# Performance work log

Hardware: AMD Instinct MI355X
Metric: run time of the kernel (lower is better)

## Reference

```python
import jax, jax.numpy as jnp
import numpy as np

DIM = 2048; H = 16; DK = 128; DV = 128; SEQ = 2048; KCONV = 4
KEY_DIM = H * DK; VAL_DIM = H * DV
EPS_L2 = 1e-6; EPS_RMS = 1e-6; SP_THRESH = 20.0


def setup_inputs() -> dict:
    key = jax.random.key(0)
    ks = jax.random.split(key, 20)
    f = jnp.float32
    def w(k, shape, scale):
        return jax.random.normal(k, shape, f) * scale
    s_in = DIM ** -0.5
    return {
        "x": jax.random.normal(ks[0], (1, SEQ, DIM), f),
        "ve": jax.random.normal(ks[1], (1, SEQ, H, DV), f),
        "sa_lambdas": jnp.array([0.7, 0.3], f),
        "Wq": w(ks[2], (DIM, KEY_DIM), s_in),
        "Wk": w(ks[3], (DIM, KEY_DIM), s_in),
        "Wv": w(ks[4], (DIM, VAL_DIM), s_in),
        "conv_q": w(ks[5], (KEY_DIM, KCONV), 0.5),
        "conv_k": w(ks[6], (KEY_DIM, KCONV), 0.5),
        "conv_v": w(ks[7], (VAL_DIM, KCONV), 0.5),
        "Wf1": w(ks[8], (DIM, DV), s_in),
        "Wf2": w(ks[9], (DV, KEY_DIM), DV ** -0.5),
        "Wb": w(ks[10], (DIM, H), s_in),
        "A_log": jnp.log(jax.random.uniform(ks[11], (H,), f, 1.0, 16.0)),
        "dt_bias": jnp.zeros((KEY_DIM,), f),
        "Wg1": w(ks[12], (DIM, DV), s_in),
        "Wg2": w(ks[13], (DV, VAL_DIM), DV ** -0.5),
        "bg2": jnp.zeros((VAL_DIM,), f),
        "norm_w": jnp.ones((DV,), f),
        "Wo": w(ks[14], (VAL_DIM, DIM), VAL_DIM ** -0.5),
    }


def _short_conv_silu(u, w):
    # u: [b, s, c], w: [c, K]; causal depthwise conv + silu
    s = u.shape[1]
    up = jnp.pad(u, ((0, 0), (w.shape[1] - 1, 0), (0, 0)))
    y = sum(up[:, i:i + s, :] * w[:, i] for i in range(w.shape[1]))
    return jax.nn.silu(y)


def _l2norm(t):
    return t * jax.lax.rsqrt(jnp.sum(t * t, axis=-1, keepdims=True) + EPS_L2)


def _forward(x, ve, sa_lambdas, Wq, Wk, Wv, conv_q, conv_k, conv_v,
             Wf1, Wf2, Wb, A_log, dt_bias, Wg1, Wg2, bg2, norm_w, Wo):
    b, s, _ = x.shape  # b == 1
    q = _short_conv_silu(x @ Wq, conv_q).reshape(b, s, H, DK)
    k = _short_conv_silu(x @ Wk, conv_k).reshape(b, s, H, DK)
    v = _short_conv_silu(x @ Wv, conv_v).reshape(b, s, H, DV)
    v = sa_lambdas[0] * v + sa_lambdas[1] * ve
    # KDA gate: per-(head, key-dim) log decay
    g = ((x @ Wf1) @ Wf2).reshape(b, s, H, DK) + dt_bias.reshape(H, DK)
    sp = jnp.where(g > SP_THRESH, g, jnp.log1p(jnp.exp(jnp.minimum(g, SP_THRESH))))
    glog = -jnp.exp(A_log)[None, None, :, None] * sp  # [b,s,h,dk]
    beta = jax.nn.sigmoid(x @ Wb)  # [b,s,h]
    # l2-normalize q,k; scale q by dk^-0.5 (chunk_kda default scale)
    qn = _l2norm(q) * (DK ** -0.5)
    kn = _l2norm(k)
    # gated delta-rule recurrence over time (b==1, squeeze batch)
    def step(S, inp):
        qt, kt, vt, gt, bt = inp  # [h,dk],[h,dk],[h,dv],[h,dk],[h]
        S = S * jnp.exp(gt)[..., None]  # per-key-channel decay
        pred = jnp.einsum('hk,hkv->hv', kt, S)
        vt_new = bt[:, None] * (vt - pred)
        S = S + kt[:, :, None] * vt_new[:, None, :]
        ot = jnp.einsum('hk,hkv->hv', qt, S)
        return S, ot
    S0 = jnp.zeros((H, DK, DV), x.dtype)
    _, o = jax.lax.scan(step, S0, (qn[0], kn[0], v[0], glog[0], beta[0]))
    o = o[None]  # [1,s,h,dv]
    # sigmoid-gated RMSNorm over head_v_dim
    gate = ((x @ Wg1) @ Wg2 + bg2).reshape(b, s, H, DV)
    var = jnp.mean(o * o, axis=-1, keepdims=True)
    o = o * jax.lax.rsqrt(var + EPS_RMS) * norm_w
    o = o * jax.nn.sigmoid(gate)
    return o.reshape(b, s, VAL_DIM) @ Wo  # [1,s,dim]


def reference(x, ve, sa_lambdas, Wq, Wk, Wv, conv_q, conv_k, conv_v,
              Wf1, Wf2, Wb, A_log, dt_bias, Wg1, Wg2, bg2, norm_w, Wo):
    return _forward(x, ve, sa_lambdas, Wq, Wk, Wv, conv_q, conv_k, conv_v,
                    Wf1, Wf2, Wb, A_log, dt_bias, Wg1, Wg2, bg2, norm_w, Wo)
```

## Files before the change

### kernel.cpp

```cpp
#include <hip/hip_runtime.h>
#include <hip/hip_bf16.h>
#include <stdint.h>
#include <stddef.h>

#define SEQL 2048
#define DIMSZ 2048
#define HN 16
#define DKD 128
#define DVD 128
#define QSCALE 0.08838834764831843f

typedef __attribute__((ext_vector_type(4))) float f32x4;
typedef __attribute__((ext_vector_type(2))) float f32x2;
typedef __attribute__((ext_vector_type(8))) short bf16x8;

__device__ __forceinline__ float sigmoid_f(float x) { return 1.f / (1.f + __expf(-x)); }

#define BM 128
#define BN 128
#define BKK 64

__global__ __launch_bounds__(256) void gemm_bt(
    const __hip_bfloat16* __restrict__ A, const __hip_bfloat16* __restrict__ B,
    float* __restrict__ C, int M, int N, int lda, int ldb, int klen, int accum)
{
  __shared__ __hip_bfloat16 As[BM * BKK];
  __shared__ __hip_bfloat16 Bs[BN * BKK];
  const int tid = threadIdx.x;
  const int lane = tid & 63;
  const int w = tid >> 6;
  const int wm = w >> 1, wn = w & 1;
  const int m0 = blockIdx.y * BM, n0 = blockIdx.x * BN;
  const int l15 = lane & 15, l4 = lane >> 4;
  const int kbase = blockIdx.z * klen;

  f32x4 acc[4][4] = {};

  for (int k0 = kbase; k0 < kbase + klen; k0 += BKK) {
#pragma unroll
    for (int i = 0; i < 4; ++i) {
      const int c = (w * 4 + i) * 64 + lane;
      const int row = c >> 3;
      const int colb = (c & 7) * 8;
      __builtin_amdgcn_global_load_lds(
          (const __attribute__((address_space(1))) void*)(A + (size_t)(m0 + row) * lda + k0 + colb),
          (__attribute__((address_space(3))) void*)(As + (size_t)c * 8), 16, 0, 0);
      __builtin_amdgcn_global_load_lds(
          (const __attribute__((address_space(1))) void*)(B + (size_t)(n0 + row) * ldb + k0 + colb),
          (__attribute__((address_space(3))) void*)(Bs + (size_t)c * 8), 16, 0, 0);
    }
    __syncthreads();
#pragma unroll
    for (int kk = 0; kk < BKK; kk += 32) {
      bf16x8 af[4], bfv[4];
#pragma unroll
      for (int mi = 0; mi < 4; ++mi)
        af[mi] = *(const bf16x8*)(As + (wm * 64 + mi * 16 + l15) * BKK + kk + l4 * 8);
#pragma unroll
      for (int ni = 0; ni < 4; ++ni)
        bfv[ni] = *(const bf16x8*)(Bs + (wn * 64 + ni * 16 + l15) * BKK + kk + l4 * 8);
#pragma unroll
      for (int mi = 0; mi < 4; ++mi)
#pragma unroll
        for (int ni = 0; ni < 4; ++ni)
          acc[mi][ni] = __builtin_amdgcn_mfma_f32_16x16x32_bf16(af[mi], bfv[ni], acc[mi][ni], 0, 0, 0);
    }
    __syncthreads();
  }

  float* Cz = C + (size_t)blockIdx.z * M * N;
#pragma unroll
  for (int mi = 0; mi < 4; ++mi) {
#pragma unroll
    for (int ni = 0; ni < 4; ++ni) {
      const int row = m0 + wm * 64 + mi * 16 + l4 * 4;
      const int col = n0 + wn * 64 + ni * 16 + l15;
#pragma unroll
      for (int r = 0; r < 4; ++r) {
        size_t idx = (size_t)(row + r) * N + col;
        if (accum) Cz[idx] += acc[mi][ni][r];
        else Cz[idx] = acc[mi][ni][r];
      }
    }
  }
}

#define PHASE256(MQ, NQ, NEEDA, NEEDB)                                          \
  {                                                                             \
    if (NEEDA) {                                                                \
      _Pragma("unroll") for (int m2 = 0; m2 < 4; ++m2)                          \
      _Pragma("unroll") for (int ks = 0; ks < 2; ++ks) {                        \
        const int la = (MQ) * 128 + wm * 64 + m2 * 16 + l15;                    \
        const int kc = ks * 4 + l4;                                             \
        a[m2][ks] = *(const bf16x8*)(lds + cb + la * 64 + (kc ^ (la & 7)) * 8); \
      }                                                                         \
    }                                                                           \
    if (NEEDB) {                                                                \
      _Pragma("unroll") for (int n2 = 0; n2 < 2; ++n2)                          \
      _Pragma("unroll") for (int ks = 0; ks < 2; ++ks) {                        \
        const int lb = (NQ) * 128 + wn * 32 + n2 * 16 + l15;                    \
        const int kc = ks * 4 + l4;                                             \
        b[n2][ks] = *(const bf16x8*)(lds + cb + 16384 + lb * 64 + (kc ^ (lb & 7)) * 8); \
      }                                                                         \
    }                                                                           \
    __builtin_amdgcn_s_setprio(1);                                              \
    _Pragma("unroll") for (int m2 = 0; m2 < 4; ++m2)                            \
    _Pragma("unroll") for (int n2 = 0; n2 < 2; ++n2)                            \
    _Pragma("unroll") for (int ks = 0; ks < 2; ++ks)                            \
      acc[(MQ) * 4 + m2][(NQ) * 2 + n2] = __builtin_amdgcn_mfma_f32_16x16x32_bf16( \
          a[m2][ks], b[n2][ks], acc[(MQ) * 4 + m2][(NQ) * 2 + n2], 0, 0, 0);    \
    __builtin_amdgcn_s_setprio(0);                                              \
  }

__global__ __launch_bounds__(512, 2) void gemm_bt256(
    const __hip_bfloat16* __restrict__ A, const __hip_bfloat16* __restrict__ B,
    float* __restrict__ C, int M, int N, int lda, int ldb, int NT)
{
  __shared__ __hip_bfloat16 lds[65536];
  const int tid = threadIdx.x;
  const int w = tid >> 6, lane = tid & 63;
  const int wm = w >> 2, wn = w & 3;
  const int l15 = lane & 15, l4 = lane >> 4;
  const int m0 = blockIdx.y * 256, n0 = blockIdx.x * 256;

  f32x4 acc[8][4] = {};
  bf16x8 a[4][2], b[2][2];

  auto stage_half = [&](int which, int t1) {
    const int buf = t1 & 1;
    const int k0n = ((t1 < NT) ? t1 : 0) * 64;
    const int mat = which & 1;
    const int half = which >> 1;
#pragma unroll
    for (int i = 0; i < 2; ++i) {
      const int c = i * 512 + tid;
      const int l = half * 128 + (c >> 3);
      const int kcs = (c & 7) ^ (l & 7);
      const __hip_bfloat16* src;
      if (mat == 0) {
        const int grow = ((l >> 6) & 1) * 128 + (l >> 7) * 64 + (l & 63);
        src = A + (size_t)(m0 + grow) * lda + k0n + kcs * 8;
      } else {
        const int gcol = ((l >> 5) & 3) * 64 + (l >> 7) * 32 + (l & 31);
        src = B + (size_t)(n0 + gcol) * ldb + k0n + kcs * 8;
      }
      __builtin_amdgcn_global_load_lds(
          (const __attribute__((address_space(1))) void*)src,
          (__attribute__((address_space(3))) void*)(lds + (size_t)buf * 32768 + mat * 16384 + half * 8192 + (size_t)c * 8),
          16, 0, 0);
    }
  };

  stage_half(0, 0); stage_half(1, 0); stage_half(2, 0); stage_half(3, 0);

  for (int t = 0; t < NT; ++t) {
    const size_t cb = (size_t)(t & 1) * 32768;
    stage_half(0, t + 1);
    asm volatile("s_waitcnt vmcnt(6)" ::: "memory");
    __builtin_amdgcn_s_barrier();
    __builtin_amdgcn_sched_barrier(0);
    PHASE256(0, 0, 1, 1)
    __builtin_amdgcn_s_barrier();
    stage_half(1, t + 1);
    asm volatile("s_waitcnt vmcnt(4)" ::: "memory");
    __builtin_amdgcn_s_barrier();
    __builtin_amdgcn_sched_barrier(0);
    PHASE256(0, 1, 0, 1)
    __builtin_amdgcn_s_barrier();
    stage_half(2, t + 1);
    __builtin_amdgcn_s_barrier();
    __builtin_amdgcn_sched_barrier(0);
    PHASE256(1, 1, 1, 0)
    __builtin_amdgcn_s_barrier();
    stage_half(3, t + 1);
    __builtin_amdgcn_s_barrier();
    __builtin_amdgcn_sched_barrier(0);
    PHASE256(1, 0, 0, 1)
    __builtin_amdgcn_s_barrier();
  }
  asm volatile("s_waitcnt vmcnt(0)" ::: "memory");

#pragma unroll
  for (int mi = 0; mi < 8; ++mi) {
#pragma unroll
    for (int ni = 0; ni < 4; ++ni) {
      const int row = m0 + wm * 128 + mi * 16 + l4 * 4;
      const int col = n0 + wn * 64 + ni * 16 + l15;
#pragma unroll
      for (int r = 0; r < 4; ++r)
        C[(size_t)(row + r) * N + col] = acc[mi][ni][r];
    }
  }
}

__global__ __launch_bounds__(256) void gemm_btsplit(
    const __hip_bfloat16* __restrict__ Ah, const __hip_bfloat16* __restrict__ Al,
    const __hip_bfloat16* __restrict__ Bh, const __hip_bfloat16* __restrict__ Bl,
    float* __restrict__ C, int M, int N, int lda, int ldb, int klen)
{
  __shared__ __hip_bfloat16 Ash[BM * BKK];
  __shared__ __hip_bfloat16 Asl[BM * BKK];
  __shared__ __hip_bfloat16 Bsh[BN * BKK];
  __shared__ __hip_bfloat16 Bsl[BN * BKK];
  const int tid = threadIdx.x;
  const int lane = tid & 63;
  const int w = tid >> 6;
  const int wm = w >> 1, wn = w & 1;
  const int m0 = blockIdx.y * BM, n0 = blockIdx.x * BN;
  const int l15 = lane & 15, l4 = lane >> 4;
  const int kbase = blockIdx.z * klen;

  f32x4 acc[4][4] = {};

  for (int k0 = kbase; k0 < kbase + klen; k0 += BKK) {
#pragma unroll
    for (int i = 0; i < 4; ++i) {
      const int c = (w * 4 + i) * 64 + lane;
      const int row = c >> 3;
      const int colb = (c & 7) * 8;
      const size_t go = (size_t)(m0 + row) * lda + k0 + colb;
      const size_t gn = (size_t)(n0 + row) * ldb + k0 + colb;
      __builtin_amdgcn_global_load_lds(
          (const __attribute__((address_space(1))) void*)(Ah + go),
          (__attribute__((address_space(3))) void*)(Ash + (size_t)c * 8), 16, 0, 0);
      __builtin_amdgcn_global_load_lds(
          (const __attribute__((address_space(1))) void*)(Al + go),
          (__attribute__((address_space(3))) void*)(Asl + (size_t)c * 8), 16, 0, 0);
      __builtin_amdgcn_global_load_lds(
          (const __attribute__((address_space(1))) void*)(Bh + gn),
          (__attribute__((address_space(3))) void*)(Bsh + (size_t)c * 8), 16, 0, 0);
      __builtin_amdgcn_global_load_lds(
          (const __attribute__((address_space(1))) void*)(Bl + gn),
          (__attribute__((address_space(3))) void*)(Bsl + (size_t)c * 8), 16, 0, 0);
    }
    __syncthreads();
#pragma unroll
    for (int kk = 0; kk < BKK; kk += 32) {
      bf16x8 afh[4], afl[4], bfh[4], bfl[4];
#pragma unroll
      for (int mi = 0; mi < 4; ++mi) {
        const int ao = (wm * 64 + mi * 16 + l15) * BKK + kk + l4 * 8;
        afh[mi] = *(const bf16x8*)(Ash + ao);
        afl[mi] = *(const bf16x8*)(Asl + ao);
      }
#pragma unroll
      for (int ni = 0; ni < 4; ++ni) {
        const int bo = (wn * 64 + ni * 16 + l15) * BKK + kk + l4 * 8;
        bfh[ni] = *(const bf16x8*)(Bsh + bo);
        bfl[ni] = *(const bf16x8*)(Bsl + bo);
      }
#pragma unroll
      for (int mi = 0; mi < 4; ++mi)
#pragma unroll
        for (int ni = 0; ni < 4; ++ni) {
          acc[mi][ni] = __builtin_amdgcn_mfma_f32_16x16x32_bf16(afh[mi], bfh[ni], acc[mi][ni], 0, 0, 0);
          acc[mi][ni] = __builtin_amdgcn_mfma_f32_16x16x32_bf16(afh[mi], bfl[ni], acc[mi][ni], 0, 0, 0);
          acc[mi][ni] = __builtin_amdgcn_mfma_f32_16x16x32_bf16(afl[mi], bfh[ni], acc[mi][ni], 0, 0, 0);
        }
    }
    __syncthreads();
  }

  float* Cz = C + (size_t)blockIdx.z * M * N;
#pragma unroll
  for (int mi = 0; mi < 4; ++mi) {
#pragma unroll
    for (int ni = 0; ni < 4; ++ni) {
      const int row = m0 + wm * 64 + mi * 16 + l4 * 4;
      const int col = n0 + wn * 64 + ni * 16 + l15;
#pragma unroll
      for (int r = 0; r < 4; ++r)
        Cz[(size_t)(row + r) * N + col] = acc[mi][ni][r];
    }
  }
}

__global__ __launch_bounds__(256) void transpose_cast_kernel(
    const float* __restrict__ in, __hip_bfloat16* __restrict__ outT,
    __hip_bfloat16* __restrict__ outLo, int R, int C)
{
  __shared__ float tile[32][33];
  const int c0 = blockIdx.x * 32, r0 = blockIdx.y * 32;
  const int tc = threadIdx.x & 31, tr = threadIdx.x >> 5;
#pragma unroll
  for (int i = 0; i < 4; ++i)
    tile[tr + i * 8][tc] = in[(size_t)(r0 + tr + i * 8) * C + c0 + tc];
  __syncthreads();
#pragma unroll
  for (int i = 0; i < 4; ++i) {
    float val = tile[tc][tr + i * 8];
    __hip_bfloat16 h = __float2bfloat16(val);
    size_t oi = (size_t)(c0 + tr + i * 8) * R + r0 + tc;
    outT[oi] = h;
    if (outLo) outLo[oi] = __float2bfloat16(val - __bfloat162float(h));
  }
}

__global__ __launch_bounds__(256) void cast_split_kernel(
    const float* __restrict__ in, __hip_bfloat16* __restrict__ hi,
    __hip_bfloat16* __restrict__ lo, int n4)
{
  int idx = blockIdx.x * 256 + threadIdx.x;
  if (idx >= n4) return;
  f32x4 v = *(const f32x4*)(in + (size_t)idx * 4);
  union { __hip_bfloat16 b[4]; unsigned long long u; } ph, pl;
#pragma unroll
  for (int j = 0; j < 4; ++j) {
    float f = v[j];
    __hip_bfloat16 hh = __float2bfloat16(f);
    ph.b[j] = hh;
    pl.b[j] = __float2bfloat16(f - __bfloat162float(hh));
  }
  *(unsigned long long*)((char*)hi + (size_t)idx * 8) = ph.u;
  if (lo) *(unsigned long long*)((char*)lo + (size_t)idx * 8) = pl.u;
}

__global__ __launch_bounds__(256) void reduce8_kernel(
    const float* __restrict__ part, __hip_bfloat16* __restrict__ hi,
    __hip_bfloat16* __restrict__ lo, int n4, size_t chunk)
{
  int idx = blockIdx.x * 256 + threadIdx.x;
  if (idx >= n4) return;
  f32x4 a = *(const f32x4*)(part + (size_t)idx * 4);
#pragma unroll
  for (int z = 1; z < 8; ++z) {
    f32x4 b = *(const f32x4*)(part + z * chunk + (size_t)idx * 4);
    a.x += b.x; a.y += b.y; a.z += b.z; a.w += b.w;
  }
  union { __hip_bfloat16 b[4]; unsigned long long u; } ph, pl;
#pragma unroll
  for (int j = 0; j < 4; ++j) {
    float f = a[j];
    __hip_bfloat16 hh = __float2bfloat16(f);
    ph.b[j] = hh;
    pl.b[j] = __float2bfloat16(f - __bfloat162float(hh));
  }
  *(unsigned long long*)((char*)hi + (size_t)idx * 8) = ph.u;
  if (lo) *(unsigned long long*)((char*)lo + (size_t)idx * 8) = pl.u;
}

__global__ __launch_bounds__(256) void beta_kernel(
    const float* __restrict__ x, const float* __restrict__ Wb, float* __restrict__ betaT)
{
  int idx = blockIdx.x * 256 + threadIdx.x;
  int s = idx >> 4, h = idx & 15;
  const float* xr = x + (size_t)s * DIMSZ;
  float acc = 0.f;
  for (int d = 0; d < DIMSZ; d += 4) {
    f32x4 xv = *(const f32x4*)(xr + d);
    acc = fmaf(xv.x, Wb[(size_t)(d + 0) * HN + h], acc);
    acc = fmaf(xv.y, Wb[(size_t)(d + 1) * HN + h], acc);
    acc = fmaf(xv.z, Wb[(size_t)(d + 2) * HN + h], acc);
    acc = fmaf(xv.w, Wb[(size_t)(d + 3) * HN + h], acc);
  }
  betaT[(size_t)h * SEQL + s] = 1.f / (1.f + expf(-acc));
}

#define SL20(r, d) ((r) * 160 + ((d) >> 4) * 20 + ((d) & 15))

__global__ __launch_bounds__(256) void kda_pref(
    const float* __restrict__ qkv, const float* __restrict__ ve,
    const float* __restrict__ lam,
    const float* __restrict__ cwq, const float* __restrict__ cwk, const float* __restrict__ cwv,
    const float* __restrict__ gbuf,
    const float* __restrict__ dtb, const float* __restrict__ A_log,
    const float* __restrict__ betaT,
    __hip_bfloat16* __restrict__ Xgh, __hip_bfloat16* __restrict__ KTh,
    float* __restrict__ uvS, float* __restrict__ olocS, float* __restrict__ Pg)
{
  __shared__ float GL2[32 * 160];
  __shared__ float kL2[32 * 160];
  __shared__ float qL2[32 * 132];
  __shared__ float vL2[32 * 128];
  __shared__ float ALB[32][33];
  __shared__ float Bdiag[32], betaL[32];
  __shared__ float csumW[4 * 128];

  const int bid = blockIdx.x;
  const int h = bid >> 6, cc = bid & 63;
  const int tid = threadIdx.x;
  const int w = tid >> 6, lane = tid & 63;
  const size_t hc = (size_t)h * 64 + cc;
  const float Aexp = __expf(A_log[h]);

  {
    const int c = lane * 2;
    const int r0g = cc * 32 + w * 8;
    const int cg = h * 128 + c;

    f32x4 wq0 = *(const f32x4*)(cwq + (size_t)cg * 4), wq1 = *(const f32x4*)(cwq + (size_t)(cg + 1) * 4);
    f32x4 wk0 = *(const f32x4*)(cwk + (size_t)cg * 4), wk1 = *(const f32x4*)(cwk + (size_t)(cg + 1) * 4);
    f32x4 wv0 = *(const f32x4*)(cwv + (size_t)cg * 4), wv1 = *(const f32x4*)(cwv + (size_t)(cg + 1) * 4);
    f32x2 dt2 = *(const f32x2*)(dtb + cg);
    const float l0 = lam[0], l1 = lam[1];

    f32x2 xqr[11], xkr[11], xvr[11];
#pragma unroll
    for (int i = 0; i < 11; ++i) {
      const int sr = r0g - 3 + i;
      if (sr >= 0) {
        const size_t ro = (size_t)sr * 6144 + cg;
        xqr[i] = *(const f32x2*)(qkv + ro);
        xkr[i] = *(const f32x2*)(qkv + 2048 + ro);
        xvr[i] = *(const f32x2*)(qkv + 4096 + ro);
      } else {
        xqr[i].x = xqr[i].y = xkr[i].x = xkr[i].y = xvr[i].x = xvr[i].y = 0.f;
      }
    }

    float gl0[8], gl1[8];
#pragma unroll
    for (int i = 0; i < 8; ++i) {
      const int rr = r0g + i;
      const int lr = w * 8 + i;
      float aq0 = 0, aq1 = 0, ak0 = 0, ak1 = 0, av0 = 0, av1 = 0;
#pragma unroll
      for (int j = 0; j < 4; ++j) {
        aq0 = fmaf(xqr[i + j].x, wq0[j], aq0); aq1 = fmaf(xqr[i + j].y, wq1[j], aq1);
        ak0 = fmaf(xkr[i + j].x, wk0[j], ak0); ak1 = fmaf(xkr[i + j].y, wk1[j], ak1);
        av0 = fmaf(xvr[i + j].x, wv0[j], av0); av1 = fmaf(xvr[i + j].y, wv1[j], av1);
      }
      float yq0 = aq0 * sigmoid_f(aq0), yq1 = aq1 * sigmoid_f(aq1);
      float yk0 = ak0 * sigmoid_f(ak0), yk1 = ak1 * sigmoid_f(ak1);
      float yv0 = av0 * sigmoid_f(av0), yv1 = av1 * sigmoid_f(av1);

      f32x2 vev = *(const f32x2*)(ve + ((size_t)rr * HN + h) * 128 + c);
      float v0 = l0 * yv0 + l1 * vev.x;
      float v1 = l0 * yv1 + l1 * vev.y;

      float ssq = yq0 * yq0 + yq1 * yq1;
      float ssk = yk0 * yk0 + yk1 * yk1;
#pragma unroll
      for (int off = 32; off > 0; off >>= 1) {
        ssq += __shfl_xor(ssq, off);
        ssk += __shfl_xor(ssk, off);
      }
      float rq = rsqrtf(ssq + 1e-6f) * QSCALE;
      float rk = rsqrtf(ssk + 1e-6f);

      f32x2 kk; kk.x = yk0 * rk; kk.y = yk1 * rk;
      f32x2 qq; qq.x = yq0 * rq; qq.y = yq1 * rq;
      f32x2 vv; vv.x = v0; vv.y = v1;
      *(f32x2*)&kL2[SL20(lr, c)] = kk;
      *(f32x2*)&qL2[lr * 132 + c] = qq;
      *(f32x2*)&vL2[lr * 128 + c] = vv;

      f32x2 gv = *(const f32x2*)(gbuf + (size_t)rr * 2048 + cg);
      float g0 = gv.x + dt2.x, g1 = gv.y + dt2.y;
      float sp0 = (g0 > 20.f) ? g0 : log1pf(__expf(fminf(g0, 20.f)));
      float sp1 = (g1 > 20.f) ? g1 : log1pf(__expf(fminf(g1, 20.f)));
      gl0[i] = -Aexp * sp0;
      gl1[i] = -Aexp * sp1;
    }
    {
      float r0 = 0.f, r1 = 0.f;
#pragma unroll
      for (int i = 0; i < 8; ++i) { r0 += gl0[i]; gl0[i] = r0; r1 += gl1[i]; gl1[i] = r1; }
      csumW[w * 128 + c] = r0;
      csumW[w * 128 + c + 1] = r1;
    }
    if (tid < 32) betaL[tid] = betaT[(size_t)h * SEQL + cc * 32 + tid];
    __syncthreads();
    {
      float p0 = 0.f, p1 = 0.f;
      for (int wp = 0; wp < w; ++wp) { p0 += csumW[wp * 128 + c]; p1 += csumW[wp * 128 + c + 1]; }
#pragma unroll
      for (int i = 0; i < 8; ++i) {
        f32x2 gg; gg.x = gl0[i] + p0; gg.y = gl1[i] + p1;
        *(f32x2*)&GL2[SL20(w * 8 + i, c)] = gg;
      }
    }
  }
  __syncthreads();

  {
    const int tg = lane >> 3, s8 = lane & 7;
    const int tt = w * 8 + tg;
    const int ds = s8 * 20;

    float Gt[16], kt[16], qt[16];
#pragma unroll
    for (int j = 0; j < 16; j += 4) {
      *(f32x4*)&Gt[j] = *(const f32x4*)&GL2[tt * 160 + ds + j];
      *(f32x4*)&kt[j] = *(const f32x4*)&kL2[tt * 160 + ds + j];
      *(f32x4*)&qt[j] = *(const f32x4*)&qL2[tt * 132 + s8 * 16 + j];
    }
    {
      float sA = 0.f, sB = 0.f;
#pragma unroll
      for (int j = 0; j < 16; ++j) { sA = fmaf(kt[j], kt[j], sA); sB = fmaf(qt[j], kt[j], sB); }
      sA += __shfl_xor(sA, 1); sA += __shfl_xor(sA, 2); sA += __shfl_xor(sA, 4);
      sB += __shfl_xor(sB, 1); sB += __shfl_xor(sB, 2); sB += __shfl_xor(sB, 4);
      if (s8 == 0) { ALB[tt][tt] = sA; Bdiag[tt] = sB; }
    }
    const int ibound = w * 8 + 7;
    for (int i = 0; i < ibound; ++i) {
      if (i < tt) {
        float sA = 0.f, sB = 0.f;
#pragma unroll
        for (int jj = 0; jj < 4; ++jj) {
          f32x4 Gi = *(const f32x4*)&GL2[i * 160 + ds + jj * 4];
          f32x4 ki = *(const f32x4*)&kL2[i * 160 + ds + jj * 4];
#pragma unroll
          for (int u = 0; u < 4; ++u) {
            float e = __expf(Gt[jj * 4 + u] - Gi[u]);
            float kid = ki[u] * e;
            sA = fmaf(kt[jj * 4 + u], kid, sA);
            sB = fmaf(qt[jj * 4 + u], kid, sB);
          }
        }
        sA += __shfl_xor(sA, 1); sA += __shfl_xor(sA, 2); sA += __shfl_xor(sA, 4);
        sB += __shfl_xor(sB, 1); sB += __shfl_xor(sB, 2); sB += __shfl_xor(sB, 4);
        if (s8 == 0) { ALB[tt][i] = sA; ALB[i][tt] = sB; }
      }
    }
  }
  __syncthreads();

  const int col = tid & 127, half = tid >> 7;
  const size_t rowbase = (size_t)(cc * 32) * 2048 + h * 128 + col;
  const int rbase = half * 16;
  {
    const float g31 = GL2[SL20(31, col)];
    size_t kb = hc * 4096 + (size_t)col * 32;
#pragma unroll
    for (int i = 0; i < 16; ++i) {
      int r = rbase + i;
      float kv = kL2[SL20(r, col)] * __expf(g31 - GL2[SL20(r, col)]);
      KTh[kb + r] = __float2bfloat16(kv);
    }
  }

  if (half == 0) {
    float expg[32];
#pragma unroll
    for (int r = 0; r < 32; ++r) expg[r] = __expf(GL2[SL20(r, col)]);

    float uvr[32], wr[32];
#pragma unroll
    for (int r = 0; r < 32; ++r) {
      float suv = 0.f, sw = 0.f;
#pragma unroll
      for (int j = 0; j < 32; ++j) {
        if (j < r) { float a = ALB[r][j]; suv = fmaf(a, uvr[j], suv); sw = fmaf(a, wr[j], sw); }
      }
      float br = betaL[r];
      float khr = kL2[SL20(r, col)] * expg[r];
      uvr[r] = br * (vL2[r * 128 + col] - suv);
      wr[r] = br * (khr - sw);
      uvS[rowbase + (size_t)r * 2048] = uvr[r];
      Xgh[hc * 8192 + (size_t)(32 + r) * 128 + col] = __float2bfloat16(wr[r]);
    }

#pragma unroll
    for (int r = 0; r < 32; ++r) {
      float qtv = qL2[r * 132 + col] * expg[r];
      float ol = 0.f;
#pragma unroll
      for (int j = 0; j < 32; ++j) {
        if (j < r) { float b = ALB[j][r]; qtv = fmaf(-b, wr[j], qtv); ol = fmaf(b, uvr[j], ol); }
      }
      { float b = Bdiag[r]; qtv = fmaf(-b, wr[r], qtv); ol = fmaf(b, uvr[r], ol); }
      Xgh[hc * 8192 + (size_t)r * 128 + col] = __float2bfloat16(qtv);
      olocS[rowbase + (size_t)r * 2048] = ol;
    }
    Pg[hc * 128 + col] = expg[31];
  }
}

#define STP 136
#define UTP 40

struct ChunkOps {
  bf16x8 ah[4];
  bf16x8 kah[2];
  f32x4 pvv[2];
  float pB[4];
};

__global__ __launch_bounds__(256) void kda_seq(
    const __hip_bfloat16* __restrict__ Xgh, const __hip_bfloat16* __restrict__ KTh,
    const float* __restrict__ uvS, const float* __restrict__ olocS,
    const float* __restrict__ Pg, float* __restrict__ obuf)
{
  __shared__ __hip_bfloat16 STh[16 * STP], STl[16 * STP];
  __shared__ __hip_bfloat16 UTh[16 * UTP];
  const int tid = threadIdx.x;
  const int w = tid >> 6, lane = tid & 63, l15 = lane & 15, l4 = lane >> 4;
  const int h = blockIdx.x >> 3, vq = blockIdx.x & 7;
  const int v0 = vq * 16;
  const int r0 = (w & 1) * 16 + l4 * 4;
  const int isO = (w < 2);

  for (int i = tid; i < 16 * STP; i += 256) {
    STh[i] = __float2bfloat16(0.f);
    STl[i] = __float2bfloat16(0.f);
  }
  __syncthreads();

  f32x4 S[2] = {};

  auto loadops = [&](ChunkOps& o, int c) {
    const size_t hc = (size_t)h * 64 + c;
    const __hip_bfloat16* xh = Xgh + hc * 8192 + (size_t)(w * 16 + l15) * 128 + l4 * 8;
#pragma unroll
    for (int kk = 0; kk < 4; ++kk) o.ah[kk] = *(const bf16x8*)(xh + kk * 32);
    const float* pb = (isO ? olocS : uvS) + (size_t)(c * 32 + r0) * 2048 + h * 128 + v0 + l15;
#pragma unroll
    for (int r = 0; r < 4; ++r) o.pB[r] = pb[(size_t)r * 2048];
#pragma unroll
    for (int mi = 0; mi < 2; ++mi) {
      const int kd = (w * 2 + mi) * 16;
      o.kah[mi] = *(const bf16x8*)(KTh + hc * 4096 + (size_t)(kd + l15) * 32 + l4 * 8);
      o.pvv[mi] = *(const f32x4*)(Pg + hc * 128 + kd + l4 * 4);
    }
  };

  auto body = [&](ChunkOps& o, int c) {
    f32x4 Y = {};
#pragma unroll
    for (int kk = 0; kk < 4; ++kk) {
      const int so = l15 * STP + kk * 32 + l4 * 8;
      bf16x8 bh = *(const bf16x8*)(STh + so);
      bf16x8 bl = *(const bf16x8*)(STl + so);
      Y = __builtin_amdgcn_mfma_f32_16x16x32_bf16(o.ah[kk], bh, Y, 0, 0, 0);
      Y = __builtin_amdgcn_mfma_f32_16x16x32_bf16(o.ah[kk], bl, Y, 0, 0, 0);
    }

    if (isO) {
      size_t ob = (size_t)(c * 32 + r0) * 2048 + h * 128 + v0 + l15;
#pragma unroll
      for (int r = 0; r < 4; ++r)
        obuf[ob + (size_t)r * 2048] = Y[r] + o.pB[r];
    } else {
      union { __hip_bfloat16 b[4]; unsigned long long u; } uh;
#pragma unroll
      for (int r = 0; r < 4; ++r)
        uh.b[r] = __float2bfloat16(o.pB[r] - Y[r]);
      *(unsigned long long*)(UTh + l15 * UTP + r0) = uh.u;
    }
    __syncthreads();

#pragma unroll
    for (int mi = 0; mi < 2; ++mi) S[mi] *= o.pvv[mi];
    {
      bf16x8 ubh = *(const bf16x8*)(UTh + l15 * UTP + l4 * 8);
#pragma unroll
      for (int mi = 0; mi < 2; ++mi)
        S[mi] = __builtin_amdgcn_mfma_f32_16x16x32_bf16(o.kah[mi], ubh, S[mi], 0, 0, 0);
    }

#pragma unroll
    for (int mi = 0; mi < 2; ++mi) {
      const int kd0 = (w * 2 + mi) * 16 + l4 * 4;
      union { __hip_bfloat16 b[4]; unsigned long long u; } sh, sl;
#pragma unroll
      for (int r = 0; r < 4; ++r) {
        __hip_bfloat16 hh = __float2bfloat16(S[mi][r]);
        sh.b[r] = hh;
        sl.b[r] = __float2bfloat16(S[mi][r] - __bfloat162float(hh));
      }
      *(unsigned long long*)(STh + l15 * STP + kd0) = sh.u;
      *(unsigned long long*)(STl + l15 * STP + kd0) = sl.u;
    }
    __syncthreads();
  };

  ChunkOps A_, B_;
  loadops(A_, 0);
  for (int c = 0; c < 64; c += 2) {
    loadops(B_, c + 1);
    body(A_, c);
    if (c + 2 < 64) loadops(A_, c + 2);
    body(B_, c + 1);
  }
}

__global__ __launch_bounds__(256) void rmsgate_kernel(
    const float* __restrict__ o, const float* __restrict__ gate,
    const float* __restrict__ bg2, const float* __restrict__ norm_w,
    __hip_bfloat16* __restrict__ og)
{
  int row = blockIdx.x * 4 + (threadIdx.x >> 6);
  int lane = threadIdx.x & 63;
  int s = row >> 4, h = row & 15;
  int j = lane * 2;
  const float* p = o + (size_t)row * 128 + j;
  f32x2 v = *(const f32x2*)p;
  float ss = v.x * v.x + v.y * v.y;
#pragma unroll
  for (int off = 32; off > 0; off >>= 1) ss += __shfl_xor(ss, off);
  float rs = rsqrtf(ss * (1.f / 128.f) + 1e-6f);
  int c = h * 128 + j;
  float g0 = gate[(size_t)s * 2048 + c] + bg2[c];
  float g1 = gate[(size_t)s * 2048 + c + 1] + bg2[c + 1];
  float o0 = v.x * rs * norm_w[j] * (1.f / (1.f + expf(-g0)));
  float o1 = v.y * rs * norm_w[j + 1] * (1.f / (1.f + expf(-g1)));
  union { __hip_bfloat16 b[2]; unsigned int u; } pk2;
  pk2.b[0] = __float2bfloat16(o0);
  pk2.b[1] = __float2bfloat16(o1);
  *(unsigned int*)((char*)og + ((size_t)s * 2048 + c) * 2) = pk2.u;
}

extern "C" void kernel_launch(void* const* d_in, const int* in_sizes, int n_in,
                              void* d_out, int out_size, void* d_ws, size_t ws_size,
                              hipStream_t stream)
{
  const float* x      = (const float*)d_in[0];
  const float* ve     = (const float*)d_in[1];
  const float* lam    = (const float*)d_in[2];
  const float* Wq     = (const float*)d_in[3];
  const float* Wk     = (const float*)d_in[4];
  const float* Wv     = (const float*)d_in[5];
  const float* cwq    = (const float*)d_in[6];
  const float* cwk    = (const float*)d_in[7];
  const float* cwv    = (const float*)d_in[8];
  const float* Wf1    = (const float*)d_in[9];
  const float* Wf2    = (const float*)d_in[10];
  const float* Wb     = (const float*)d_in[11];
  const float* A_log  = (const float*)d_in[12];
  const float* dtb    = (const float*)d_in[13];
  const float* Wg1    = (const float*)d_in[14];
  const float* Wg2    = (const float*)d_in[15];
  const float* bg2    = (const float*)d_in[16];
  const float* norm_w = (const float*)d_in[17];
  const float* Wo     = (const float*)d_in[18];
  float* out = (float*)d_out;

  const size_t S2 = (size_t)2048 * 2048;

  char* p = (char*)d_ws;
  auto alloc = [&](size_t bytes) { char* r = p; p += (bytes + 255) & ~(size_t)255; return r; };

  __hip_bfloat16* xb     = (__hip_bfloat16*)alloc(S2 * 2);
  __hip_bfloat16* WoT    = (__hip_bfloat16*)alloc(S2 * 2);
  __hip_bfloat16* Wf2hT  = (__hip_bfloat16*)alloc(2048 * 128 * 2);
  __hip_bfloat16* Wf2lT  = (__hip_bfloat16*)alloc(2048 * 128 * 2);
  __hip_bfloat16* Wg2T   = (__hip_bfloat16*)alloc(2048 * 128 * 2);
  __hip_bfloat16* Wfg1hT = (__hip_bfloat16*)alloc((size_t)256 * 2048 * 2);
  __hip_bfloat16* Wfg1lT = (__hip_bfloat16*)alloc((size_t)256 * 2048 * 2);
  __hip_bfloat16* f1g1h  = (__hip_bfloat16*)alloc((size_t)2048 * 256 * 2);
  __hip_bfloat16* f1g1l  = (__hip_bfloat16*)alloc((size_t)2048 * 256 * 2);
  float* betaT = (float*)alloc((size_t)2048 * 16 * 4);
  float* qkv   = (float*)alloc(3 * S2 * 4);
  float* gbuf  = (float*)alloc(S2 * 4);
  float* gatebuf = (float*)alloc(S2 * 4);
  float* uvS   = (float*)alloc(S2 * 4);
  float* olocS = (float*)alloc(S2 * 4);
  __hip_bfloat16* Xgh = (__hip_bfloat16*)alloc(S2 * 4);
  __hip_bfloat16* KTh = (__hip_bfloat16*)alloc(S2 * 2);
  float* Pg    = (float*)alloc((size_t)1024 * 128 * 4);

  __hip_bfloat16* WqkvT = (__hip_bfloat16*)uvS;
  __hip_bfloat16* xlo = (__hip_bfloat16*)((char*)olocS + S2 * 2);
  float* fpart = (float*)Xgh;
  float* obuf  = gbuf;
  __hip_bfloat16* og = (__hip_bfloat16*)qkv;

  cast_split_kernel<<<4096, 256, 0, stream>>>(x, xb, xlo, (int)(S2 / 4));

  transpose_cast_kernel<<<dim3(64, 64), 256, 0, stream>>>(Wq, WqkvT, nullptr, 2048, 2048);
  transpose_cast_kernel<<<dim3(64, 64), 256, 0, stream>>>(Wk, WqkvT + 2048 * 2048, nullptr, 2048, 2048);
  transpose_cast_kernel<<<dim3(64, 64), 256, 0, stream>>>(Wv, WqkvT + 2 * 2048 * 2048, nullptr, 2048, 2048);
  transpose_cast_kernel<<<dim3(64, 64), 256, 0, stream>>>(Wo, WoT, nullptr, 2048, 2048);
  transpose_cast_kernel<<<dim3(4, 64), 256, 0, stream>>>(Wf1, Wfg1hT, Wfg1lT, 2048, 128);
  transpose_cast_kernel<<<dim3(4, 64), 256, 0, stream>>>(Wg1, Wfg1hT + 128 * 2048, nullptr, 2048, 128);
  hipMemsetAsync(Wfg1lT + 128 * 2048, 0, (size_t)128 * 2048 * 2, stream);
  transpose_cast_kernel<<<dim3(64, 4), 256, 0, stream>>>(Wf2, Wf2hT, Wf2lT, 128, 2048);
  transpose_cast_kernel<<<dim3(64, 4), 256, 0, stream>>>(Wg2, Wg2T, nullptr, 128, 2048);

  gemm_bt256<<<dim3(24, 8), 512, 0, stream>>>(xb, WqkvT, qkv, 2048, 6144, 2048, 2048, 32);

  gemm_btsplit<<<dim3(2, 16, 8), 256, 0, stream>>>(xb, xlo, Wfg1hT, Wfg1lT, fpart,
                                                   2048, 256, 2048, 2048, 256);
  reduce8_kernel<<<512, 256, 0, stream>>>(fpart, f1g1h, f1g1l, 131072, (size_t)2048 * 256);

  gemm_btsplit<<<dim3(16, 16), 256, 0, stream>>>(f1g1h, f1g1l, Wf2hT, Wf2lT, gbuf,
                                                 2048, 2048, 256, 128, 128);
  gemm_bt<<<dim3(16, 16), 256, 0, stream>>>(f1g1h + 128, Wg2T, gatebuf,
                                            2048, 2048, 256, 128, 128, 0);

  beta_kernel<<<128, 256, 0, stream>>>(x, Wb, betaT);

  kda_pref<<<1024, 256, 0, stream>>>(qkv, ve, lam, cwq, cwk, cwv, gbuf, dtb, A_log, betaT,
                                     Xgh, KTh, uvS, olocS, Pg);

  kda_seq<<<128, 256, 0, stream>>>(Xgh, KTh, uvS, olocS, Pg, obuf);

  rmsgate_kernel<<<8192, 256, 0, stream>>>(obuf, gatebuf, bg2, norm_w, og);

  gemm_bt<<<dim3(16, 16), 256, 0, stream>>>(og, WoT, out, 2048, 2048, 2048, 2048, 2048, 0);
}
```

Baseline: 402.7 us.

## Use split-K 256-tile GEMM for output projection, bf16 intermediates, rebalance pref rows

The final Wo projection moves from the 128-tile gemm_bt to the pipelined 256-tile gemm_bt256 with a two-way split-K over blockIdx.z, followed by a small reduction kernel that sums the two partial outputs. The uvS and olocS intermediates are stored in bf16 instead of fp32, halving their memory traffic at some cost in precision. The kda_pref pairwise loop now interleaves time rows across waves so the triangular work is spread more evenly. The split-K adds an extra 32MB round trip for the partials and a kernel launch.

```diff
diff --git a/kernel.cpp b/kernel.cpp
--- a/kernel.cpp
+++ b/kernel.cpp
@@ -122,13 +122,14 @@
   const int wm = w >> 2, wn = w & 3;
   const int l15 = lane & 15, l4 = lane >> 4;
   const int m0 = blockIdx.y * 256, n0 = blockIdx.x * 256;
+  const int kb0 = blockIdx.z * NT;
 
   f32x4 acc[8][4] = {};
   bf16x8 a[4][2], b[2][2];
 
   auto stage_half = [&](int which, int t1) {
     const int buf = t1 & 1;
-    const int k0n = ((t1 < NT) ? t1 : 0) * 64;
+    const int k0n = (kb0 + ((t1 < NT) ? t1 : 0)) * 64;
     const int mat = which & 1;
     const int half = which >> 1;
 #pragma unroll
@@ -180,6 +181,7 @@
   }
   asm volatile("s_waitcnt vmcnt(0)" ::: "memory");
 
+  float* Cz = C + (size_t)blockIdx.z * M * N;
 #pragma unroll
   for (int mi = 0; mi < 8; ++mi) {
 #pragma unroll
@@ -188,9 +190,21 @@
       const int col = n0 + wn * 64 + ni * 16 + l15;
 #pragma unroll
       for (int r = 0; r < 4; ++r)
-        C[(size_t)(row + r) * N + col] = acc[mi][ni][r];
-    }
-  }
+        Cz[(size_t)(row + r) * N + col] = acc[mi][ni][r];
+    }
+  }
+}
+
+__global__ __launch_bounds__(256) void reduce2_kernel(
+    const float* __restrict__ part, float* __restrict__ out, int n4)
+{
+  int idx = blockIdx.x * 256 + threadIdx.x;
+  if (idx >= n4) return;
+  const size_t chunk = (size_t)SEQL * DIMSZ;
+  f32x4 a = *(const f32x4*)(part + (size_t)idx * 4);
+  f32x4 b = *(const f32x4*)(part + chunk + (size_t)idx * 4);
+  a.x += b.x; a.y += b.y; a.z += b.z; a.w += b.w;
+  *(f32x4*)(out + (size_t)idx * 4) = a;
 }
 
 __global__ __launch_bounds__(256) void gemm_btsplit(
@@ -366,7 +380,8 @@
     const float* __restrict__ dtb, const float* __restrict__ A_log,
     const float* __restrict__ betaT,
     __hip_bfloat16* __restrict__ Xgh, __hip_bfloat16* __restrict__ KTh,
-    float* __restrict__ uvS, float* __restrict__ olocS, float* __restrict__ Pg)
+    __hip_bfloat16* __restrict__ uvS, __hip_bfloat16* __restrict__ olocS,
+    float* __restrict__ Pg)
 {
   __shared__ float GL2[32 * 160];
   __shared__ float kL2[32 * 160];
@@ -475,7 +490,7 @@
 
   {
     const int tg = lane >> 3, s8 = lane & 7;
-    const int tt = w * 8 + tg;
+    const int tt = w + 4 * tg;
     const int ds = s8 * 20;
 
     float Gt[16], kt[16], qt[16];
@@ -493,7 +508,7 @@
       sB += __shfl_xor(sB, 1); sB += __shfl_xor(sB, 2); sB += __shfl_xor(sB, 4);
       if (s8 == 0) { ALB[tt][tt] = sA; Bdiag[tt] = sB; }
     }
-    const int ibound = w * 8 + 7;
+    const int ibound = 28 + w;
     for (int i = 0; i < ibound; ++i) {
       if (i < tt) {
         float sA = 0.f, sB = 0.f;
@@ -548,7 +563,7 @@
       float khr = kL2[SL20(r, col)] * expg[r];
       uvr[r] = br * (vL2[r * 128 + col] - suv);
       wr[r] = br * (khr - sw);
-      uvS[rowbase + (size_t)r * 2048] = uvr[r];
+      uvS[rowbase + (size_t)r * 2048] = __float2bfloat16(uvr[r]);
       Xgh[hc * 8192 + (size_t)(32 + r) * 128 + col] = __float2bfloat16(wr[r]);
     }
 
@@ -562,7 +577,7 @@
       }
       { float b = Bdiag[r]; qtv = fmaf(-b, wr[r], qtv); ol = fmaf(b, uvr[r], ol); }
       Xgh[hc * 8192 + (size_t)r * 128 + col] = __float2bfloat16(qtv);
-      olocS[rowbase + (size_t)r * 2048] = ol;
+      olocS[rowbase + (size_t)r * 2048] = __float2bfloat16(ol);
     }
     Pg[hc * 128 + col] = expg[31];
   }
@@ -580,7 +595,7 @@
 
 __global__ __launch_bounds__(256) void kda_seq(
     const __hip_bfloat16* __restrict__ Xgh, const __hip_bfloat16* __restrict__ KTh,
-    const float* __restrict__ uvS, const float* __restrict__ olocS,
+    const __hip_bfloat16* __restrict__ uvS, const __hip_bfloat16* __restrict__ olocS,
     const float* __restrict__ Pg, float* __restrict__ obuf)
 {
   __shared__ __hip_bfloat16 STh[16 * STP], STl[16 * STP];
@@ -605,9 +620,9 @@
     const __hip_bfloat16* xh = Xgh + hc * 8192 + (size_t)(w * 16 + l15) * 128 + l4 * 8;
 #pragma unroll
     for (int kk = 0; kk < 4; ++kk) o.ah[kk] = *(const bf16x8*)(xh + kk * 32);
-    const float* pb = (isO ? olocS : uvS) + (size_t)(c * 32 + r0) * 2048 + h * 128 + v0 + l15;
-#pragma unroll
-    for (int r = 0; r < 4; ++r) o.pB[r] = pb[(size_t)r * 2048];
+    const __hip_bfloat16* pb = (isO ? olocS : uvS) + (size_t)(c * 32 + r0) * 2048 + h * 128 + v0 + l15;
+#pragma unroll
+    for (int r = 0; r < 4; ++r) o.pB[r] = __bfloat162float(pb[(size_t)r * 2048]);
 #pragma unroll
     for (int mi = 0; mi < 2; ++mi) {
       const int kd = (w * 2 + mi) * 16;
@@ -745,8 +760,8 @@
   float* qkv   = (float*)alloc(3 * S2 * 4);
   float* gbuf  = (float*)alloc(S2 * 4);
   float* gatebuf = (float*)alloc(S2 * 4);
-  float* uvS   = (float*)alloc(S2 * 4);
-  float* olocS = (float*)alloc(S2 * 4);
+  __hip_bfloat16* uvS   = (__hip_bfloat16*)alloc(S2 * 4);
+  __hip_bfloat16* olocS = (__hip_bfloat16*)alloc(S2 * 4);
   __hip_bfloat16* Xgh = (__hip_bfloat16*)alloc(S2 * 4);
   __hip_bfloat16* KTh = (__hip_bfloat16*)alloc(S2 * 2);
   float* Pg    = (float*)alloc((size_t)1024 * 128 * 4);
@@ -756,6 +771,7 @@
   float* fpart = (float*)Xgh;
   float* obuf  = gbuf;
   __hip_bfloat16* og = (__hip_bfloat16*)qkv;
+  float* wpart = (float*)((char*)qkv + 16 * 1024 * 1024);
 
   cast_split_kernel<<<4096, 256, 0, stream>>>(x, xb, xlo, (int)(S2 / 4));
 
@@ -769,7 +785,7 @@
   transpose_cast_kernel<<<dim3(64, 4), 256, 0, stream>>>(Wf2, Wf2hT, Wf2lT, 128, 2048);
   transpose_cast_kernel<<<dim3(64, 4), 256, 0, stream>>>(Wg2, Wg2T, nullptr, 128, 2048);
 
-  gemm_bt256<<<dim3(24, 8), 512, 0, stream>>>(xb, WqkvT, qkv, 2048, 6144, 2048, 2048, 32);
+  gemm_bt256<<<dim3(24, 8, 1), 512, 0, stream>>>(xb, WqkvT, qkv, 2048, 6144, 2048, 2048, 32);
 
   gemm_btsplit<<<dim3(2, 16, 8), 256, 0, stream>>>(xb, xlo, Wfg1hT, Wfg1lT, fpart,
                                                    2048, 256, 2048, 2048, 256);
@@ -789,5 +805,6 @@
 
   rmsgate_kernel<<<8192, 256, 0, stream>>>(obuf, gatebuf, bg2, norm_w, og);
 
-  gemm_bt<<<dim3(16, 16), 256, 0, stream>>>(og, WoT, out, 2048, 2048, 2048, 2048, 2048, 0);
-}
+  gemm_bt256<<<dim3(8, 8, 2), 512, 0, stream>>>(og, WoT, wpart, 2048, 2048, 2048, 2048, 16);
+  reduce2_kernel<<<4096, 256, 0, stream>>>(wpart, out, (int)(S2 / 4));
+}
```

After: 409.0 us. About the same (+1.6%).
